# Kernel optimization log

Measured on AMD Instinct MI355X. Metric: run time of the kernel, lower is better.

## Reference

```python
import jax, jax.numpy as jnp
import numpy as np

NUM_CLASSES = 5
VDIM = 16
IN_CH = 512
B, H, W = 32, 64, 64
LEVEL_OFFSETS = [0, 2, 5, 9]  # flat offsets of levels 1..4 (2,3,4,5 nodes)


def conv1x1(x, w, b):
    # x: [B,C,H,W], w: [O,C], b: [O] -> [B,O,H,W]
    return jnp.einsum('bchw,oc->bohw', x, w) + b[None, :, None, None]


def setup_inputs() -> dict:
    key = jax.random.key(0)
    ks = jax.random.split(key, 8)
    features = jax.random.normal(ks[0], (B, IN_CH, H, W), dtype=jnp.float32)
    # He init (fan_out = out_channels for 1x1 convs), biases zero
    root_w = jax.random.normal(ks[1], (VDIM, IN_CH), dtype=jnp.float32) * np.sqrt(2.0 / VDIM)
    root_b = jnp.zeros((VDIM,), jnp.float32)
    level_w = jax.random.normal(ks[2], (14, VDIM, VDIM), dtype=jnp.float32) * np.sqrt(2.0 / VDIM)
    level_b = jnp.zeros((14, VDIM), jnp.float32)
    m1_w = jax.random.normal(ks[3], (64, VDIM), dtype=jnp.float32) * np.sqrt(2.0 / 64.0)
    m1_b = jnp.zeros((64,), jnp.float32)
    m2_w = jax.random.normal(ks[4], (1, 64), dtype=jnp.float32) * np.sqrt(2.0 / 1.0)
    m2_b = jnp.zeros((1,), jnp.float32)
    return dict(features=features, root_w=root_w, root_b=root_b,
                level_w=level_w, level_b=level_b,
                m1_w=m1_w, m1_b=m1_b, m2_w=m2_w, m2_b=m2_b)


def reference(features, root_w, root_b, level_w, level_b, m1_w, m1_b, m2_w, m2_b):
    b = features.shape[0]
    feats = [conv1x1(features, root_w, root_b)]  # level 0: root, [B,VDIM,H,W]
    for level in range(1, NUM_CLASSES):
        off = LEVEL_OFFSETS[level - 1]
        num_nodes = level + 1
        nxt = []
        for node in range(num_nodes):
            pl = max(0, node - 1)
            pr = min(node, level - 1)
            if pl == pr:
                parent = feats[pl]
            else:
                # L2 norm of GAP-pooled parent vectors; pick larger-norm parent
                ln = jnp.linalg.norm(feats[pl].mean(axis=(2, 3)), axis=1)  # [B]
                rn = jnp.linalg.norm(feats[pr].mean(axis=(2, 3)), axis=1)
                sel = (rn > ln).astype(features.dtype)[:, None, None, None]
                parent = feats[pl] * (1.0 - sel) + feats[pr] * sel
            nxt.append(conv1x1(parent, level_w[off + node], level_b[off + node]))
        feats = nxt
    # leaves: NUM_CLASSES tensors [B,VDIM,H,W]
    leaf_pooled = jnp.stack([f.mean(axis=(2, 3)) for f in feats], axis=1)  # [B,K,VDIM]
    class_logits = jnp.linalg.norm(leaf_pooled, axis=2)                    # [B,K]
    selected_class = jnp.argmax(class_logits, axis=1)                      # [B]
    leaf_stack = jnp.stack(feats, axis=1)                                  # [B,K,VDIM,H,W]
    sel_idx = selected_class[:, None, None, None, None]
    selected_feat = jnp.take_along_axis(leaf_stack, sel_idx, axis=1)[:, 0]  # [B,VDIM,H,W]
    feat_norm = jnp.linalg.norm(selected_feat, axis=1, keepdims=True) + 1e-8
    normalized = selected_feat / feat_norm
    m1 = jax.nn.relu(conv1x1(normalized, m1_w, m1_b))
    m2 = conv1x1(m1, m2_w, m2_b)                 # [B,1,H,W]
    mantissa_raw = m2.mean(axis=(2, 3))[:, 0]    # [B]
    mantissa = jax.nn.sigmoid(mantissa_raw) * 0.75 + 0.75
    return (class_logits, mantissa, selected_class)
```

## Files before the change

### kernel.cpp

```cpp
#include <hip/hip_runtime.h>
#include <math.h>

#define HW 4096
#define NB 32
#define VD 16

#define OFF_M0P   0
#define OFF_MSP   8192
#define OFF_M     8448
#define OFF_C     16640
#define OFF_WT    17152
#define OFF_CNT   25344
#define OFF_P     25408

__global__ __launch_bounds__(256) void k_trans(const float* __restrict__ rw,
                                               float* __restrict__ wt) {
    int i = blockIdx.x * 256 + threadIdx.x;
    if (i < 512 * VD) {
        int c = i >> 4, o = i & 15;
        wt[i] = rw[o * 512 + c];
    }
}

__global__ __launch_bounds__(256) void k_root(const float* __restrict__ feat,
                                              const float* __restrict__ wt,
                                              const float* __restrict__ rb,
                                              float* __restrict__ f0,
                                              float* __restrict__ m0p) {
    const int b  = blockIdx.y;
    const int bx = blockIdx.x;
    const int t  = threadIdx.x;
    const int px = bx * 256 + t;
    const float* fp = feat + (size_t)b * 512 * HW + px;

    float acc[VD];
#pragma unroll
    for (int o = 0; o < VD; ++o) acc[o] = rb[o];

    float cur[8], nxt[8];
#pragma unroll
    for (int k = 0; k < 8; ++k) cur[k] = fp[(size_t)k * HW];

    for (int c = 0; c < 512; c += 8) {
        if (c + 8 < 512) {
#pragma unroll
            for (int k = 0; k < 8; ++k)
                nxt[k] = fp[(size_t)(c + 8 + k) * HW];
        }
#pragma unroll
        for (int g = 0; g < 2; ++g) {
            const float* wr = wt + (size_t)(c + g * 4) * VD;
#pragma unroll
            for (int k = 0; k < 4; ++k) {
                float x = cur[g * 4 + k];
#pragma unroll
                for (int o = 0; o < VD; ++o)
                    acc[o] = fmaf(wr[k * VD + o], x, acc[o]);
            }
        }
#pragma unroll
        for (int k = 0; k < 8; ++k) cur[k] = nxt[k];
    }

    float* op = f0 + (size_t)b * VD * HW + px;
#pragma unroll
    for (int o = 0; o < VD; ++o) op[(size_t)o * HW] = acc[o];

    __shared__ float red[4][VD];
    const int lane = t & 63, wv = t >> 6;
#pragma unroll
    for (int o = 0; o < VD; ++o) {
        float v = acc[o];
#pragma unroll
        for (int off = 32; off > 0; off >>= 1) v += __shfl_down(v, off);
        if (lane == 0) red[wv][o] = v;
    }
    __syncthreads();
    if (t < VD)
        m0p[(b * 16 + bx) * VD + t] =
            red[0][t] + red[1][t] + red[2][t] + red[3][t];
}

__global__ __launch_bounds__(64) void k_tree(const float* __restrict__ lw,
                                             const float* __restrict__ lb,
                                             float* __restrict__ ws,
                                             float* __restrict__ out) {
    const int b = blockIdx.x;
    const int t = threadIdx.x;
    if (b == 0 && t == 0) *(int*)(ws + OFF_CNT) = 0;

    __shared__ float lm[15][VD];
    __shared__ float Wst[256];
    __shared__ int   path[5];
    const int Soff[5] = {0, 1, 3, 6, 10};
    const int LOFF[4] = {0, 2, 5, 9};

    if (t < VD) {
        float s = 0.f;
        for (int k = 0; k < 16; ++k) s += ws[OFF_M0P + (b * 16 + k) * VD + t];
        lm[0][t] = s * (1.0f / HW);
    }
    __syncthreads();

    for (int l = 1; l <= 4; ++l) {
        if (t < VD) {
            for (int n = 0; n <= l; ++n) {
                int pl = (n - 1 < 0) ? 0 : (n - 1);
                int pr = (n < l - 1) ? n : (l - 1);
                const float* A = lm[Soff[l - 1] + pl];
                const float* R = lm[Soff[l - 1] + pr];
                bool takeR = false;
                if (pl != pr) {
                    float ln = 0.f, rn = 0.f;
                    for (int k = 0; k < VD; ++k) { ln += A[k] * A[k]; rn += R[k] * R[k]; }
                    takeR = sqrtf(rn) > sqrtf(ln);
                }
                int widx = LOFF[l - 1] + n;
                float s = lb[widx * VD + t];
                for (int k = 0; k < VD; ++k) {
                    float pk = takeR ? R[k] : A[k];
                    s += lw[(widx * VD + t) * VD + k] * pk;
                }
                lm[Soff[l] + n][t] = s;
            }
        }
        __syncthreads();
    }

    if (t == 0) {
        float best = -1.f; int bi = 0;
        for (int n = 0; n < 5; ++n) {
            float s = 0.f;
            for (int k = 0; k < VD; ++k) { float v = lm[10 + n][k]; s += v * v; }
            float lg = sqrtf(s);
            out[b * 5 + n] = lg;
            if (lg > best) { best = lg; bi = n; }
        }
        out[192 + b] = (float)bi;
        int node = bi;
        for (int l = 4; l >= 1; --l) {
            path[l] = LOFF[l - 1] + node;
            int pl = (node - 1 < 0) ? 0 : (node - 1);
            int pr = (node < l - 1) ? node : (l - 1);
            if (pl == pr) node = pl;
            else {
                float ln = 0.f, rn = 0.f;
                for (int k = 0; k < VD; ++k) {
                    float a = lm[Soff[l - 1] + pl][k], r = lm[Soff[l - 1] + pr][k];
                    ln += a * a; rn += r * r;
                }
                node = (sqrtf(rn) > sqrtf(ln)) ? pr : pl;
            }
        }
    }
    __syncthreads();

    for (int i = t; i < 256; i += 64) Wst[i] = lw[path[1] * 256 + i];
    __syncthreads();
    float Mc[VD], cc[VD];
    if (t < VD) {
        for (int i = 0; i < VD; ++i) Mc[i] = Wst[i * VD + t];
        for (int i = 0; i < VD; ++i) cc[i] = lb[path[1] * VD + i];
    }
    for (int l = 2; l <= 4; ++l) {
        __syncthreads();
        for (int i = t; i < 256; i += 64) Wst[i] = lw[path[l] * 256 + i];
        __syncthreads();
        if (t < VD) {
            float nM[VD], nc[VD];
            for (int i = 0; i < VD; ++i) {
                float sm = 0.f, sc = 0.f;
                for (int k = 0; k < VD; ++k) {
                    float w = Wst[i * VD + k];
                    sm += w * Mc[k]; sc += w * cc[k];
                }
                nM[i] = sm; nc[i] = sc + lb[path[l] * VD + i];
            }
            for (int i = 0; i < VD; ++i) { Mc[i] = nM[i]; cc[i] = nc[i]; }
        }
    }
    if (t < VD) {
        for (int i = 0; i < VD; ++i) ws[OFF_M + b * 256 + i * VD + t] = Mc[i];
        if (t == 0) for (int i = 0; i < VD; ++i) ws[OFF_C + b * VD + i] = cc[i];
    }
}

__global__ __launch_bounds__(256) void k_final(const float* __restrict__ f0,
                                               const float* __restrict__ Mg,
                                               const float* __restrict__ Cg,
                                               const float* __restrict__ m1w,
                                               const float* __restrict__ m1b,
                                               const float* __restrict__ m2w,
                                               const float* __restrict__ m2b,
                                               float* __restrict__ msp,
                                               int* __restrict__ cnt,
                                               float* __restrict__ out) {
    const int b = blockIdx.y;
    const int t = threadIdx.x;
    __shared__ float sM[256], sc[VD], s1w[1024], s1b[64], s2w[64];
    __shared__ int lastflag;
    sM[t] = Mg[b * 256 + t];
    for (int i = t; i < 1024; i += 256) s1w[i] = m1w[i];
    if (t < 64) { s1b[t] = m1b[t]; s2w[t] = m2w[t]; }
    if (t < VD) sc[t] = Cg[b * VD + t];
    __syncthreads();

    const size_t base = (size_t)b * VD * HW + blockIdx.x * 512 + t * 2;
    float2 f[VD];
#pragma unroll
    for (int j = 0; j < VD; ++j)
        f[j] = *(const float2*)(f0 + base + (size_t)j * HW);

    float2 v[VD];
#pragma unroll
    for (int i = 0; i < VD; ++i) {
        float2 s; s.x = s.y = sc[i];
#pragma unroll
        for (int j = 0; j < VD; ++j) {
            float w = sM[i * VD + j];
            s.x += w * f[j].x; s.y += w * f[j].y;
        }
        v[i] = s;
    }

    float2 n2; n2.x = n2.y = 0.f;
#pragma unroll
    for (int i = 0; i < VD; ++i) { n2.x += v[i].x * v[i].x; n2.y += v[i].y * v[i].y; }
    float2 inv;
    inv.x = 1.f / (sqrtf(n2.x) + 1e-8f);
    inv.y = 1.f / (sqrtf(n2.y) + 1e-8f);
#pragma unroll
    for (int i = 0; i < VD; ++i) { v[i].x *= inv.x; v[i].y *= inv.y; }

    float mb = m2b[0];
    float2 s2; s2.x = s2.y = mb;
#pragma unroll 8
    for (int o = 0; o < 64; ++o) {
        float2 h; h.x = h.y = s1b[o];
#pragma unroll
        for (int i = 0; i < VD; ++i) {
            float w = s1w[o * VD + i];
            h.x += w * v[i].x; h.y += w * v[i].y;
        }
        h.x = fmaxf(h.x, 0.f); h.y = fmaxf(h.y, 0.f);
        float w2 = s2w[o];
        s2.x += w2 * h.x; s2.y += w2 * h.y;
    }
    float psum = s2.x + s2.y;

    const int lane = t & 63, wv = t >> 6;
#pragma unroll
    for (int off = 32; off > 0; off >>= 1) psum += __shfl_down(psum, off);
    __shared__ float rs[4];
    if (lane == 0) rs[wv] = psum;
    __syncthreads();
    if (t == 0) {
        msp[b * 8 + blockIdx.x] = rs[0] + rs[1] + rs[2] + rs[3];
        __threadfence();
        int old = atomicAdd(cnt, 1);
        lastflag = (old == NB * 8 - 1);
    }
    __syncthreads();

    if (lastflag) {
        __threadfence();
        if (t < NB) {
            const volatile float* vmsp = msp;
            float m = 0.f;
            for (int k = 0; k < 8; ++k) m += vmsp[t * 8 + k];
            m *= (1.0f / HW);
            out[160 + t] = (1.0f / (1.0f + expf(-m))) * 0.75f + 0.75f;
        }
    }
}

extern "C" void kernel_launch(void* const* d_in, const int* in_sizes, int n_in,
                              void* d_out, int out_size, void* d_ws, size_t ws_size,
                              hipStream_t stream) {
    const float* feat    = (const float*)d_in[0];
    const float* root_w  = (const float*)d_in[1];
    const float* root_b  = (const float*)d_in[2];
    const float* level_w = (const float*)d_in[3];
    const float* level_b = (const float*)d_in[4];
    const float* m1w     = (const float*)d_in[5];
    const float* m1b     = (const float*)d_in[6];
    const float* m2w     = (const float*)d_in[7];
    const float* m2b     = (const float*)d_in[8];
    float* ws  = (float*)d_ws;
    float* out = (float*)d_out;

    k_trans<<<32, 256, 0, stream>>>(root_w, ws + OFF_WT);
    k_root<<<dim3(16, NB), 256, 0, stream>>>(feat, ws + OFF_WT, root_b,
                                             ws + OFF_P, ws + OFF_M0P);
    k_tree<<<NB, 64, 0, stream>>>(level_w, level_b, ws, out);
    k_final<<<dim3(8, NB), 256, 0, stream>>>(ws + OFF_P, ws + OFF_M, ws + OFF_C,
                                             m1w, m1b, m2w, m2b, ws + OFF_MSP,
                                             (int*)(ws + OFF_CNT), out);
}
```

Baseline: 411.9 us.

## Fuse root conv, tree walk and mantissa head into one kernel with per-batch barrier

Merges the root 1x1 conv, the per-batch tree reduction and the final normalize/MLP head into a single kernel. Blocks of the same batch synchronize through a per-batch atomic counter spin-wait, so the root conv output stays in registers and is never written to or re-read from global memory. Every block redundantly recomputes the tree composite matrix. This relies on all 16 blocks of a batch being co-resident (512 blocks at two per CU) and risks deadlock or stalls if that does not hold.

```diff
diff --git a/kernel.cpp b/kernel.cpp
--- a/kernel.cpp
+++ b/kernel.cpp
@@ -7,31 +7,52 @@
 
 #define OFF_M0P   0
 #define OFF_MSP   8192
-#define OFF_M     8448
-#define OFF_C     16640
-#define OFF_WT    17152
-#define OFF_CNT   25344
-#define OFF_P     25408
-
-__global__ __launch_bounds__(256) void k_trans(const float* __restrict__ rw,
-                                               float* __restrict__ wt) {
+#define OFF_WT    8704
+#define OFF_CNT   16896
+
+#define LD_AGENT(p)     __hip_atomic_load((p), __ATOMIC_RELAXED, __HIP_MEMORY_SCOPE_AGENT)
+#define ST_AGENT(p, v)  __hip_atomic_store((p), (v), __ATOMIC_RELAXED, __HIP_MEMORY_SCOPE_AGENT)
+
+__global__ __launch_bounds__(256) void k_init(const float* __restrict__ rw,
+                                              float* __restrict__ ws) {
     int i = blockIdx.x * 256 + threadIdx.x;
     if (i < 512 * VD) {
         int c = i >> 4, o = i & 15;
-        wt[i] = rw[o * 512 + c];
-    }
+        ws[OFF_WT + i] = rw[o * 512 + c];
+    }
+    if (blockIdx.x == 0 && threadIdx.x < 33)
+        ((int*)(ws + OFF_CNT))[threadIdx.x] = 0;
 }
 
-__global__ __launch_bounds__(256) void k_root(const float* __restrict__ feat,
-                                              const float* __restrict__ wt,
-                                              const float* __restrict__ rb,
-                                              float* __restrict__ f0,
-                                              float* __restrict__ m0p) {
+__global__ __launch_bounds__(256, 2) void k_fused(const float* __restrict__ feat,
+                                                  const float* __restrict__ rb,
+                                                  const float* __restrict__ lw,
+                                                  const float* __restrict__ lb,
+                                                  const float* __restrict__ m1w,
+                                                  const float* __restrict__ m1b,
+                                                  const float* __restrict__ m2w,
+                                                  const float* __restrict__ m2b,
+                                                  float* __restrict__ ws,
+                                                  float* __restrict__ out) {
     const int b  = blockIdx.y;
     const int bx = blockIdx.x;
     const int t  = threadIdx.x;
     const int px = bx * 256 + t;
+
+    __shared__ float s1w[1024], s1b[64], s2w[64];
+    __shared__ float red[4][VD];
+    __shared__ float lm[15][VD];
+    __shared__ float Wst[256];
+    __shared__ float sM[256], scb[VD];
+    __shared__ float rs[4];
+    __shared__ int   path[5];
+    __shared__ int   lastflag;
+
+    for (int i = t; i < 1024; i += 256) s1w[i] = m1w[i];
+    if (t < 64) { s1b[t] = m1b[t]; s2w[t] = m2w[t]; }
+
     const float* fp = feat + (size_t)b * 512 * HW + px;
+    const float* wt = ws + OFF_WT;
 
     float acc[VD];
 #pragma unroll
@@ -62,11 +83,6 @@
         for (int k = 0; k < 8; ++k) cur[k] = nxt[k];
     }
 
-    float* op = f0 + (size_t)b * VD * HW + px;
-#pragma unroll
-    for (int o = 0; o < VD; ++o) op[(size_t)o * HW] = acc[o];
-
-    __shared__ float red[4][VD];
     const int lane = t & 63, wv = t >> 6;
 #pragma unroll
     for (int o = 0; o < VD; ++o) {
@@ -76,28 +92,30 @@
         if (lane == 0) red[wv][o] = v;
     }
     __syncthreads();
+    float* m0p = ws + OFF_M0P;
     if (t < VD)
-        m0p[(b * 16 + bx) * VD + t] =
-            red[0][t] + red[1][t] + red[2][t] + red[3][t];
-}
-
-__global__ __launch_bounds__(64) void k_tree(const float* __restrict__ lw,
-                                             const float* __restrict__ lb,
-                                             float* __restrict__ ws,
-                                             float* __restrict__ out) {
-    const int b = blockIdx.x;
-    const int t = threadIdx.x;
-    if (b == 0 && t == 0) *(int*)(ws + OFF_CNT) = 0;
-
-    __shared__ float lm[15][VD];
-    __shared__ float Wst[256];
-    __shared__ int   path[5];
+        ST_AGENT(&m0p[(b * 16 + bx) * VD + t],
+                 red[0][t] + red[1][t] + red[2][t] + red[3][t]);
+
+    int* cnt = (int*)(ws + OFF_CNT);
+    __threadfence();
+    if (t == 0) {
+        __hip_atomic_fetch_add(cnt + b, 1, __ATOMIC_RELEASE,
+                               __HIP_MEMORY_SCOPE_AGENT);
+        while (__hip_atomic_load(cnt + b, __ATOMIC_ACQUIRE,
+                                 __HIP_MEMORY_SCOPE_AGENT) < 16)
+            __builtin_amdgcn_s_sleep(2);
+    }
+    __syncthreads();
+    __threadfence();
+
     const int Soff[5] = {0, 1, 3, 6, 10};
     const int LOFF[4] = {0, 2, 5, 9};
 
     if (t < VD) {
         float s = 0.f;
-        for (int k = 0; k < 16; ++k) s += ws[OFF_M0P + (b * 16 + k) * VD + t];
+        for (int k = 0; k < 16; ++k)
+            s += LD_AGENT(&m0p[((size_t)b * 16 + k) * VD + t]);
         lm[0][t] = s * (1.0f / HW);
     }
     __syncthreads();
@@ -133,10 +151,10 @@
             float s = 0.f;
             for (int k = 0; k < VD; ++k) { float v = lm[10 + n][k]; s += v * v; }
             float lg = sqrtf(s);
-            out[b * 5 + n] = lg;
+            if (bx == 0) out[b * 5 + n] = lg;
             if (lg > best) { best = lg; bi = n; }
         }
-        out[192 + b] = (float)bi;
+        if (bx == 0) out[192 + b] = (float)bi;
         int node = bi;
         for (int l = 4; l >= 1; --l) {
             path[l] = LOFF[l - 1] + node;
@@ -155,7 +173,7 @@
     }
     __syncthreads();
 
-    for (int i = t; i < 256; i += 64) Wst[i] = lw[path[1] * 256 + i];
+    Wst[t] = lw[path[1] * 256 + t];
     __syncthreads();
     float Mc[VD], cc[VD];
     if (t < VD) {
@@ -164,110 +182,73 @@
     }
     for (int l = 2; l <= 4; ++l) {
         __syncthreads();
-        for (int i = t; i < 256; i += 64) Wst[i] = lw[path[l] * 256 + i];
+        Wst[t] = lw[path[l] * 256 + t];
         __syncthreads();
         if (t < VD) {
             float nM[VD], nc[VD];
             for (int i = 0; i < VD; ++i) {
-                float sm = 0.f, sc = 0.f;
+                float sm = 0.f, sc2 = 0.f;
                 for (int k = 0; k < VD; ++k) {
                     float w = Wst[i * VD + k];
-                    sm += w * Mc[k]; sc += w * cc[k];
-                }
-                nM[i] = sm; nc[i] = sc + lb[path[l] * VD + i];
+                    sm += w * Mc[k]; sc2 += w * cc[k];
+                }
+                nM[i] = sm; nc[i] = sc2 + lb[path[l] * VD + i];
             }
             for (int i = 0; i < VD; ++i) { Mc[i] = nM[i]; cc[i] = nc[i]; }
         }
     }
     if (t < VD) {
-        for (int i = 0; i < VD; ++i) ws[OFF_M + b * 256 + i * VD + t] = Mc[i];
-        if (t == 0) for (int i = 0; i < VD; ++i) ws[OFF_C + b * VD + i] = cc[i];
-    }
-}
-
-__global__ __launch_bounds__(256) void k_final(const float* __restrict__ f0,
-                                               const float* __restrict__ Mg,
-                                               const float* __restrict__ Cg,
-                                               const float* __restrict__ m1w,
-                                               const float* __restrict__ m1b,
-                                               const float* __restrict__ m2w,
-                                               const float* __restrict__ m2b,
-                                               float* __restrict__ msp,
-                                               int* __restrict__ cnt,
-                                               float* __restrict__ out) {
-    const int b = blockIdx.y;
-    const int t = threadIdx.x;
-    __shared__ float sM[256], sc[VD], s1w[1024], s1b[64], s2w[64];
-    __shared__ int lastflag;
-    sM[t] = Mg[b * 256 + t];
-    for (int i = t; i < 1024; i += 256) s1w[i] = m1w[i];
-    if (t < 64) { s1b[t] = m1b[t]; s2w[t] = m2w[t]; }
-    if (t < VD) sc[t] = Cg[b * VD + t];
-    __syncthreads();
-
-    const size_t base = (size_t)b * VD * HW + blockIdx.x * 512 + t * 2;
-    float2 f[VD];
-#pragma unroll
-    for (int j = 0; j < VD; ++j)
-        f[j] = *(const float2*)(f0 + base + (size_t)j * HW);
-
-    float2 v[VD];
+        for (int i = 0; i < VD; ++i) sM[i * VD + t] = Mc[i];
+        if (t == 0) for (int i = 0; i < VD; ++i) scb[i] = cc[i];
+    }
+    __syncthreads();
+
+    float v[VD];
 #pragma unroll
     for (int i = 0; i < VD; ++i) {
-        float2 s; s.x = s.y = sc[i];
-#pragma unroll
-        for (int j = 0; j < VD; ++j) {
-            float w = sM[i * VD + j];
-            s.x += w * f[j].x; s.y += w * f[j].y;
-        }
+        float s = scb[i];
+#pragma unroll
+        for (int j = 0; j < VD; ++j) s += sM[i * VD + j] * acc[j];
         v[i] = s;
     }
-
-    float2 n2; n2.x = n2.y = 0.f;
-#pragma unroll
-    for (int i = 0; i < VD; ++i) { n2.x += v[i].x * v[i].x; n2.y += v[i].y * v[i].y; }
-    float2 inv;
-    inv.x = 1.f / (sqrtf(n2.x) + 1e-8f);
-    inv.y = 1.f / (sqrtf(n2.y) + 1e-8f);
-#pragma unroll
-    for (int i = 0; i < VD; ++i) { v[i].x *= inv.x; v[i].y *= inv.y; }
-
-    float mb = m2b[0];
-    float2 s2; s2.x = s2.y = mb;
+    float n2 = 0.f;
+#pragma unroll
+    for (int i = 0; i < VD; ++i) n2 += v[i] * v[i];
+    float inv = 1.f / (sqrtf(n2) + 1e-8f);
+#pragma unroll
+    for (int i = 0; i < VD; ++i) v[i] *= inv;
+
+    float psum = m2b[0];
 #pragma unroll 8
     for (int o = 0; o < 64; ++o) {
-        float2 h; h.x = h.y = s1b[o];
-#pragma unroll
-        for (int i = 0; i < VD; ++i) {
-            float w = s1w[o * VD + i];
-            h.x += w * v[i].x; h.y += w * v[i].y;
-        }
-        h.x = fmaxf(h.x, 0.f); h.y = fmaxf(h.y, 0.f);
-        float w2 = s2w[o];
-        s2.x += w2 * h.x; s2.y += w2 * h.y;
-    }
-    float psum = s2.x + s2.y;
-
-    const int lane = t & 63, wv = t >> 6;
+        float h = s1b[o];
+#pragma unroll
+        for (int i = 0; i < VD; ++i) h += s1w[o * VD + i] * v[i];
+        h = fmaxf(h, 0.f);
+        psum += s2w[o] * h;
+    }
+
 #pragma unroll
     for (int off = 32; off > 0; off >>= 1) psum += __shfl_down(psum, off);
-    __shared__ float rs[4];
     if (lane == 0) rs[wv] = psum;
     __syncthreads();
+
+    float* msp = ws + OFF_MSP;
     if (t == 0) {
-        msp[b * 8 + blockIdx.x] = rs[0] + rs[1] + rs[2] + rs[3];
+        ST_AGENT(&msp[b * 16 + bx], rs[0] + rs[1] + rs[2] + rs[3]);
         __threadfence();
-        int old = atomicAdd(cnt, 1);
-        lastflag = (old == NB * 8 - 1);
+        int old = __hip_atomic_fetch_add(cnt + 32, 1, __ATOMIC_ACQ_REL,
+                                         __HIP_MEMORY_SCOPE_AGENT);
+        lastflag = (old == NB * 16 - 1);
     }
     __syncthreads();
 
     if (lastflag) {
         __threadfence();
         if (t < NB) {
-            const volatile float* vmsp = msp;
             float m = 0.f;
-            for (int k = 0; k < 8; ++k) m += vmsp[t * 8 + k];
+            for (int k = 0; k < 16; ++k)
+                m += LD_AGENT(&msp[t * 16 + k]);
             m *= (1.0f / HW);
             out[160 + t] = (1.0f / (1.0f + expf(-m))) * 0.75f + 0.75f;
         }
@@ -289,11 +270,7 @@
     float* ws  = (float*)d_ws;
     float* out = (float*)d_out;
 
-    k_trans<<<32, 256, 0, stream>>>(root_w, ws + OFF_WT);
-    k_root<<<dim3(16, NB), 256, 0, stream>>>(feat, ws + OFF_WT, root_b,
-                                             ws + OFF_P, ws + OFF_M0P);
-    k_tree<<<NB, 64, 0, stream>>>(level_w, level_b, ws, out);
-    k_final<<<dim3(8, NB), 256, 0, stream>>>(ws + OFF_P, ws + OFF_M, ws + OFF_C,
-                                             m1w, m1b, m2w, m2b, ws + OFF_MSP,
-                                             (int*)(ws + OFF_CNT), out);
+    k_init<<<32, 256, 0, stream>>>(root_w, ws);
+    k_fused<<<dim3(16, NB), 256, 0, stream>>>(feat, root_b, level_w, level_b,
+                                              m1w, m1b, m2w, m2b, ws, out);
 }
```

Measured after the change: 496.1 us. 20.4% more time.

## Fuse tree kernel into final kernel, recomputing tree per block

Applied to the files above, without the earlier changes.

The small per-batch tree kernel is folded into the final kernel: each of the 8 blocks per batch recomputes the level means, path and composed 16x16 matrix in shared memory, and the f0 loads are issued first so they overlap that work. This removes one kernel launch and the global round trip for M and C. The counter reset moves into the weight-transpose kernel, and the last-block reduction now uses agent-scope atomics instead of fences and volatile loads. The cost is redundant tree computation, done serially by 16 threads in every block.

```diff
diff --git a/kernel.cpp b/kernel.cpp
--- a/kernel.cpp
+++ b/kernel.cpp
@@ -7,19 +7,22 @@
 
 #define OFF_M0P   0
 #define OFF_MSP   8192
-#define OFF_M     8448
-#define OFF_C     16640
-#define OFF_WT    17152
-#define OFF_CNT   25344
-#define OFF_P     25408
-
-__global__ __launch_bounds__(256) void k_trans(const float* __restrict__ rw,
-                                               float* __restrict__ wt) {
+#define OFF_WT    8448
+#define OFF_CNT   16640
+#define OFF_P     16704
+
+#define LD_AGENT(p)     __hip_atomic_load((p), __ATOMIC_RELAXED, __HIP_MEMORY_SCOPE_AGENT)
+#define ST_AGENT(p, v)  __hip_atomic_store((p), (v), __ATOMIC_RELAXED, __HIP_MEMORY_SCOPE_AGENT)
+
+__global__ __launch_bounds__(256) void k_init(const float* __restrict__ rw,
+                                              float* __restrict__ ws) {
     int i = blockIdx.x * 256 + threadIdx.x;
     if (i < 512 * VD) {
         int c = i >> 4, o = i & 15;
-        wt[i] = rw[o * 512 + c];
-    }
+        ws[OFF_WT + i] = rw[o * 512 + c];
+    }
+    if (blockIdx.x == 0 && threadIdx.x == 0)
+        *(int*)(ws + OFF_CNT) = 0;
 }
 
 __global__ __launch_bounds__(256) void k_root(const float* __restrict__ feat,
@@ -81,23 +84,43 @@
             red[0][t] + red[1][t] + red[2][t] + red[3][t];
 }
 
-__global__ __launch_bounds__(64) void k_tree(const float* __restrict__ lw,
-                                             const float* __restrict__ lb,
-                                             float* __restrict__ ws,
-                                             float* __restrict__ out) {
-    const int b = blockIdx.x;
-    const int t = threadIdx.x;
-    if (b == 0 && t == 0) *(int*)(ws + OFF_CNT) = 0;
-
+__global__ __launch_bounds__(256) void k_final(const float* __restrict__ f0,
+                                               const float* __restrict__ lw,
+                                               const float* __restrict__ lb,
+                                               const float* __restrict__ m1w,
+                                               const float* __restrict__ m1b,
+                                               const float* __restrict__ m2w,
+                                               const float* __restrict__ m2b,
+                                               float* __restrict__ ws,
+                                               float* __restrict__ out) {
+    const int b  = blockIdx.y;
+    const int bx = blockIdx.x;
+    const int t  = threadIdx.x;
+
+    __shared__ float s1w[1024], s1b[64], s2w[64];
     __shared__ float lm[15][VD];
     __shared__ float Wst[256];
+    __shared__ float sM[256], scb[VD];
+    __shared__ float rs[4];
     __shared__ int   path[5];
+    __shared__ int   lastflag;
+
+    const size_t base = (size_t)b * VD * HW + bx * 512 + t * 2;
+    float2 f[VD];
+#pragma unroll
+    for (int j = 0; j < VD; ++j)
+        f[j] = *(const float2*)(f0 + base + (size_t)j * HW);
+
+    for (int i = t; i < 1024; i += 256) s1w[i] = m1w[i];
+    if (t < 64) { s1b[t] = m1b[t]; s2w[t] = m2w[t]; }
+
     const int Soff[5] = {0, 1, 3, 6, 10};
     const int LOFF[4] = {0, 2, 5, 9};
 
     if (t < VD) {
+        const float* mp = ws + OFF_M0P + (size_t)b * 16 * VD + t;
         float s = 0.f;
-        for (int k = 0; k < 16; ++k) s += ws[OFF_M0P + (b * 16 + k) * VD + t];
+        for (int k = 0; k < 16; ++k) s += mp[k * VD];
         lm[0][t] = s * (1.0f / HW);
     }
     __syncthreads();
@@ -133,10 +156,10 @@
             float s = 0.f;
             for (int k = 0; k < VD; ++k) { float v = lm[10 + n][k]; s += v * v; }
             float lg = sqrtf(s);
-            out[b * 5 + n] = lg;
+            if (bx == 0) out[b * 5 + n] = lg;
             if (lg > best) { best = lg; bi = n; }
         }
-        out[192 + b] = (float)bi;
+        if (bx == 0) out[192 + b] = (float)bi;
         int node = bi;
         for (int l = 4; l >= 1; --l) {
             path[l] = LOFF[l - 1] + node;
@@ -155,7 +178,7 @@
     }
     __syncthreads();
 
-    for (int i = t; i < 256; i += 64) Wst[i] = lw[path[1] * 256 + i];
+    Wst[t] = lw[path[1] * 256 + t];
     __syncthreads();
     float Mc[VD], cc[VD];
     if (t < VD) {
@@ -164,57 +187,31 @@
     }
     for (int l = 2; l <= 4; ++l) {
         __syncthreads();
-        for (int i = t; i < 256; i += 64) Wst[i] = lw[path[l] * 256 + i];
+        Wst[t] = lw[path[l] * 256 + t];
         __syncthreads();
         if (t < VD) {
             float nM[VD], nc[VD];
             for (int i = 0; i < VD; ++i) {
-                float sm = 0.f, sc = 0.f;
+                float sm = 0.f, sc2 = 0.f;
                 for (int k = 0; k < VD; ++k) {
                     float w = Wst[i * VD + k];
-                    sm += w * Mc[k]; sc += w * cc[k];
-                }
-                nM[i] = sm; nc[i] = sc + lb[path[l] * VD + i];
+                    sm += w * Mc[k]; sc2 += w * cc[k];
+                }
+                nM[i] = sm; nc[i] = sc2 + lb[path[l] * VD + i];
             }
             for (int i = 0; i < VD; ++i) { Mc[i] = nM[i]; cc[i] = nc[i]; }
         }
     }
     if (t < VD) {
-        for (int i = 0; i < VD; ++i) ws[OFF_M + b * 256 + i * VD + t] = Mc[i];
-        if (t == 0) for (int i = 0; i < VD; ++i) ws[OFF_C + b * VD + i] = cc[i];
-    }
-}
-
-__global__ __launch_bounds__(256) void k_final(const float* __restrict__ f0,
-                                               const float* __restrict__ Mg,
-                                               const float* __restrict__ Cg,
-                                               const float* __restrict__ m1w,
-                                               const float* __restrict__ m1b,
-                                               const float* __restrict__ m2w,
-                                               const float* __restrict__ m2b,
-                                               float* __restrict__ msp,
-                                               int* __restrict__ cnt,
-                                               float* __restrict__ out) {
-    const int b = blockIdx.y;
-    const int t = threadIdx.x;
-    __shared__ float sM[256], sc[VD], s1w[1024], s1b[64], s2w[64];
-    __shared__ int lastflag;
-    sM[t] = Mg[b * 256 + t];
-    for (int i = t; i < 1024; i += 256) s1w[i] = m1w[i];
-    if (t < 64) { s1b[t] = m1b[t]; s2w[t] = m2w[t]; }
-    if (t < VD) sc[t] = Cg[b * VD + t];
-    __syncthreads();
-
-    const size_t base = (size_t)b * VD * HW + blockIdx.x * 512 + t * 2;
-    float2 f[VD];
-#pragma unroll
-    for (int j = 0; j < VD; ++j)
-        f[j] = *(const float2*)(f0 + base + (size_t)j * HW);
+        for (int i = 0; i < VD; ++i) sM[i * VD + t] = Mc[i];
+        if (t == 0) for (int i = 0; i < VD; ++i) scb[i] = cc[i];
+    }
+    __syncthreads();
 
     float2 v[VD];
 #pragma unroll
     for (int i = 0; i < VD; ++i) {
-        float2 s; s.x = s.y = sc[i];
+        float2 s; s.x = s.y = scb[i];
 #pragma unroll
         for (int j = 0; j < VD; ++j) {
             float w = sM[i * VD + j];
@@ -251,23 +248,24 @@
     const int lane = t & 63, wv = t >> 6;
 #pragma unroll
     for (int off = 32; off > 0; off >>= 1) psum += __shfl_down(psum, off);
-    __shared__ float rs[4];
     if (lane == 0) rs[wv] = psum;
     __syncthreads();
+
+    float* msp = ws + OFF_MSP;
+    int* cnt = (int*)(ws + OFF_CNT);
     if (t == 0) {
-        msp[b * 8 + blockIdx.x] = rs[0] + rs[1] + rs[2] + rs[3];
-        __threadfence();
-        int old = atomicAdd(cnt, 1);
+        ST_AGENT(&msp[b * 8 + bx], rs[0] + rs[1] + rs[2] + rs[3]);
+        int old = __hip_atomic_fetch_add(cnt, 1, __ATOMIC_ACQ_REL,
+                                         __HIP_MEMORY_SCOPE_AGENT);
         lastflag = (old == NB * 8 - 1);
     }
     __syncthreads();
 
     if (lastflag) {
-        __threadfence();
         if (t < NB) {
-            const volatile float* vmsp = msp;
             float m = 0.f;
-            for (int k = 0; k < 8; ++k) m += vmsp[t * 8 + k];
+            for (int k = 0; k < 8; ++k)
+                m += LD_AGENT(&msp[t * 8 + k]);
             m *= (1.0f / HW);
             out[160 + t] = (1.0f / (1.0f + expf(-m))) * 0.75f + 0.75f;
         }
@@ -289,11 +287,9 @@
     float* ws  = (float*)d_ws;
     float* out = (float*)d_out;
 
-    k_trans<<<32, 256, 0, stream>>>(root_w, ws + OFF_WT);
+    k_init<<<32, 256, 0, stream>>>(root_w, ws);
     k_root<<<dim3(16, NB), 256, 0, stream>>>(feat, ws + OFF_WT, root_b,
-                                             ws + OFF_P, ws + OFF_M0P);
-    k_tree<<<NB, 64, 0, stream>>>(level_w, level_b, ws, out);
-    k_final<<<dim3(8, NB), 256, 0, stream>>>(ws + OFF_P, ws + OFF_M, ws + OFF_C,
-                                             m1w, m1b, m2w, m2b, ws + OFF_MSP,
-                                             (int*)(ws + OFF_CNT), out);
-}
+                                             ws + OFF_P, ws);
+    k_final<<<dim3(8, NB), 256, 0, stream>>>(ws + OFF_P, level_w, level_b,
+                                             m1w, m1b, m2w, m2b, ws, out);
+}
```

Measured after the change: 399.4 us. -3.0%, faster.
